# Kernel tuning notes

Measured on AMD Instinct MI355X. Metric: run time of the kernel, lower is better.

Reference implementation:

```python
import jax, jax.numpy as jnp
import numpy as np

DIM = 1024
HEADS = 16
DIM_HEAD = 64
INNER = HEADS * DIM_HEAD
SCALE = DIM_HEAD ** -0.5
LN_EPS = 1e-5
MASK_VALUE = -np.finfo(np.float32).max


def setup_inputs() -> dict:
    key = jax.random.key(0)
    ks = jax.random.split(key, 3)
    x = jax.random.normal(ks[0], (2, 2048, DIM), dtype=jnp.float32)
    w_qkv = jax.random.normal(ks[1], (DIM, 3 * INNER), dtype=jnp.float32) * (DIM ** -0.5)
    w_out = jax.random.normal(ks[2], (INNER, DIM), dtype=jnp.float32) * (INNER ** -0.5)
    ln_gamma = jnp.ones((DIM,), dtype=jnp.float32)
    ln_beta = jnp.zeros((DIM,), dtype=jnp.float32)
    return {"x": x, "ln_gamma": ln_gamma, "ln_beta": ln_beta, "w_qkv": w_qkv, "w_out": w_out}


def reference(x, ln_gamma, ln_beta, w_qkv, w_out):
    b, n, _ = x.shape
    # LayerNorm
    mu = jnp.mean(x, axis=-1, keepdims=True)
    var = jnp.mean(jnp.square(x - mu), axis=-1, keepdims=True)
    xn = (x - mu) * jax.lax.rsqrt(var + LN_EPS) * ln_gamma + ln_beta
    # QKV projection, split into heads: b n (h d) -> b h n d
    qkv = xn @ w_qkv  # [b, n, 3*inner]
    q, k, v = jnp.split(qkv, 3, axis=-1)
    def to_heads(t):
        return t.reshape(b, n, HEADS, DIM_HEAD).transpose(0, 2, 1, 3)
    q, k, v = to_heads(q), to_heads(k), to_heads(v)
    # scaled scores with diagonal excluded
    dots = jnp.einsum('bhnd,bhmd->bhnm', q, k) * SCALE
    eye = jnp.eye(n, dtype=bool)
    dots = jnp.where(eye, MASK_VALUE, dots)
    attn = jax.nn.softmax(dots, axis=-1)
    out = jnp.einsum('bhnm,bhmd->bhnd', attn, v)
    out = out.transpose(0, 2, 1, 3).reshape(b, n, INNER)
    return out @ w_out
```

## Files before the change

### kernel.cpp

```cpp
#include <hip/hip_runtime.h>


#define DIMM   1024
#define NSEQ   2048
#define BATCH  2
#define HEADS  16
#define DHEAD  64
#define QKVN   3072
#define MROWS  4096

typedef float          f32x4  __attribute__((ext_vector_type(4)));
typedef __bf16         bf16x8 __attribute__((ext_vector_type(8)));
typedef __bf16         bf16x4 __attribute__((ext_vector_type(4)));
typedef unsigned short u16x8  __attribute__((ext_vector_type(8)));
typedef unsigned short u16x4  __attribute__((ext_vector_type(4)));

#define QSCALE (0.125f * 1.4426950408889634f)

#if __has_builtin(__builtin_amdgcn_exp2f)
#define EXP2(x) __builtin_amdgcn_exp2f(x)
#else
#define EXP2(x) exp2f(x)
#endif

__device__ __forceinline__ unsigned short f2bf(float f) {
  unsigned u = __builtin_bit_cast(unsigned, f);
  u += 0x7FFFu + ((u >> 16) & 1u);
  return (unsigned short)(u >> 16);
}
__device__ __forceinline__ bf16x8 as_bf(u16x8 v) { return __builtin_bit_cast(bf16x8, v); }

__device__ __forceinline__ u16x4 cvt4(f32x4 v) {
  bf16x4 b;
  b[0] = (__bf16)v[0]; b[1] = (__bf16)v[1]; b[2] = (__bf16)v[2]; b[3] = (__bf16)v[3];
  return __builtin_bit_cast(u16x4, b);
}

__device__ __forceinline__ void gl_lds16(const unsigned short* g, unsigned short* l) {
  __builtin_amdgcn_global_load_lds(
      (const __attribute__((address_space(1))) unsigned*)g,
      (__attribute__((address_space(3))) unsigned*)l, 16, 0, 0);
}

__device__ __forceinline__ bf16x8 lds_frag(const unsigned short* base, int row, int chunk) {
  return as_bf(*(const u16x8*)&base[row * 64 + ((chunk ^ (row & 7)) << 3)]);
}

__device__ __forceinline__ void transpose_tile(
    const float* __restrict__ src, unsigned short* __restrict__ dst,
    int R, int C, int bx, int by, int tid) {
  __shared__ float t[32][33];
  const int rb = by * 32, cb = bx * 32;
  const int r0 = tid >> 5;
  const int c  = tid & 31;
#pragma unroll
  for (int i = 0; i < 4; ++i)
    t[r0 + i * 8][c] = src[(rb + r0 + i * 8) * C + cb + c];
  __syncthreads();
#pragma unroll
  for (int i = 0; i < 4; ++i)
    dst[(cb + r0 + i * 8) * R + rb + c] = f2bf(t[c][r0 + i * 8]);
}

__global__ __launch_bounds__(256) void prep_kernel(
    const float* __restrict__ x, const float* __restrict__ g,
    const float* __restrict__ be, const float* __restrict__ w_qkv,
    const float* __restrict__ w_out, unsigned short* __restrict__ xn,
    unsigned short* __restrict__ wqkvT, unsigned short* __restrict__ woutT) {
  const int bid = blockIdx.x, tid = threadIdx.x;
  if (bid < MROWS) {
    const int row = bid;
    const int wave = tid >> 6, lane = tid & 63;
    const float4 v = *(const float4*)&x[row * DIMM + tid * 4];
    float s  = v.x + v.y + v.z + v.w;
    float s2 = v.x * v.x + v.y * v.y + v.z * v.z + v.w * v.w;
#pragma unroll
    for (int o = 32; o >= 1; o >>= 1) { s += __shfl_xor(s, o); s2 += __shfl_xor(s2, o); }
    __shared__ float ps[4], ps2[4];
    if (lane == 0) { ps[wave] = s; ps2[wave] = s2; }
    __syncthreads();
    s  = ps[0] + ps[1] + ps[2] + ps[3];
    s2 = ps2[0] + ps2[1] + ps2[2] + ps2[3];
    const float mu  = s * (1.0f / DIMM);
    const float var = s2 * (1.0f / DIMM) - mu * mu;
    const float rs  = rsqrtf(var + 1e-5f);
    const float4 gg = *(const float4*)&g[tid * 4];
    const float4 bb = *(const float4*)&be[tid * 4];
    u16x4 o;
    o[0] = f2bf((v.x - mu) * rs * gg.x + bb.x);
    o[1] = f2bf((v.y - mu) * rs * gg.y + bb.y);
    o[2] = f2bf((v.z - mu) * rs * gg.z + bb.z);
    o[3] = f2bf((v.w - mu) * rs * gg.w + bb.w);
    *(u16x4*)&xn[row * DIMM + tid * 4] = o;
  } else {
    const int t = bid - MROWS;
    const int bx = t & 127, by = t >> 7;
    if (bx < QKVN / 32) transpose_tile(w_qkv, wqkvT, DIMM, QKVN, bx, by, tid);
    else                transpose_tile(w_out, woutT, DIMM, DIMM, bx - QKVN / 32, by, tid);
  }
}

__global__ __launch_bounds__(256, 3) void gemm_qkv_kernel(
    const unsigned short* __restrict__ A, const unsigned short* __restrict__ Bt,
    unsigned short* __restrict__ qb, unsigned short* __restrict__ kb,
    unsigned short* __restrict__ vtb) {
  __shared__ __attribute__((aligned(16))) unsigned short As[128 * 64];
  __shared__ __attribute__((aligned(16))) unsigned short Bs[128 * 64];
  const int tid = threadIdx.x;
  const int bm = blockIdx.y, bn = blockIdx.x;
  const int lane = tid & 63, wave = tid >> 6;
  const int l15 = lane & 15, quad = lane >> 4;
  const int wm = wave >> 1, wn = wave & 1;
  const int lrow = lane >> 3;
  const int gcol = ((lane & 7) ^ lrow) << 3;
  const unsigned short* Ab = A  + (bm * 128 + wave * 32 + lrow) * DIMM + gcol;
  const unsigned short* Bb = Bt + (bn * 128 + wave * 32 + lrow) * DIMM + gcol;
  const bool swap = (bn < 16);
  f32x4 acc[4][4] = {};

  for (int k0 = 0; k0 < DIMM; k0 += 64) {
#pragma unroll
    for (int j = 0; j < 4; ++j) {
      gl_lds16(Ab + j * 8 * DIMM + k0, &As[(wave * 32 + j * 8) * 64]);
      gl_lds16(Bb + j * 8 * DIMM + k0, &Bs[(wave * 32 + j * 8) * 64]);
    }
    __syncthreads();
#pragma unroll
    for (int kk = 0; kk < 2; ++kk) {
      bf16x8 af[4], bfr[4];
#pragma unroll
      for (int mi = 0; mi < 4; ++mi) af[mi]  = lds_frag(As, wm * 64 + mi * 16 + l15, kk * 4 + quad);
#pragma unroll
      for (int ni = 0; ni < 4; ++ni) bfr[ni] = lds_frag(Bs, wn * 64 + ni * 16 + l15, kk * 4 + quad);
      if (swap) {
#pragma unroll
        for (int mi = 0; mi < 4; ++mi)
#pragma unroll
          for (int ni = 0; ni < 4; ++ni)
            acc[mi][ni] = __builtin_amdgcn_mfma_f32_16x16x32_bf16(bfr[ni], af[mi], acc[mi][ni], 0, 0, 0);
      } else {
#pragma unroll
        for (int mi = 0; mi < 4; ++mi)
#pragma unroll
          for (int ni = 0; ni < 4; ++ni)
            acc[mi][ni] = __builtin_amdgcn_mfma_f32_16x16x32_bf16(af[mi], bfr[ni], acc[mi][ni], 0, 0, 0);
      }
    }
    __syncthreads();
  }

  if (swap) {
    const int colbase = bn * 128 + wn * 64;
    const int which = colbase >> 10;
    unsigned short* dst = which ? kb : qb;
    const float sc = which ? 1.0f : QSCALE;
#pragma unroll
    for (int mi = 0; mi < 4; ++mi) {
      const int m = bm * 128 + wm * 64 + mi * 16 + l15;
      const int bh0 = (m >> 11) * HEADS;
      const int n = m & 2047;
#pragma unroll
      for (int ni = 0; ni < 4; ++ni) {
        const int wc = (colbase & 1023) + ni * 16 + quad * 4;
        const int h = wc >> 6, dd = wc & 63;
        f32x4 v = acc[mi][ni] * sc;
        *(u16x4*)&dst[((bh0 + h) * NSEQ + n) * DHEAD + dd] = cvt4(v);
      }
    }
  } else {
    const int colbase = bn * 128 + wn * 64 - 2048;
#pragma unroll
    for (int mi = 0; mi < 4; ++mi) {
      const int m0 = bm * 128 + wm * 64 + mi * 16 + quad * 4;
      const int bh0 = (m0 >> 11) * HEADS;
      const int n0 = m0 & 2047;
#pragma unroll
      for (int ni = 0; ni < 4; ++ni) {
        const int vcol = colbase + ni * 16 + l15;
        const int h = vcol >> 6, dd = vcol & 63;
        *(u16x4*)&vtb[((bh0 + h) * DHEAD + dd) * NSEQ + n0] = cvt4(acc[mi][ni]);
      }
    }
  }
}

__global__ __launch_bounds__(512, 4) void attn_kernel(
    const unsigned short* __restrict__ qb, const unsigned short* __restrict__ kb,
    const unsigned short* __restrict__ vtb, unsigned short* __restrict__ attn_out) {
  __shared__ __attribute__((aligned(16))) unsigned short Ks[2][64 * 64];
  __shared__ __attribute__((aligned(16))) unsigned short Vts[2][64 * 64];
  __shared__ __attribute__((aligned(16))) unsigned short Ps[8][16][72];
  const int tid = threadIdx.x, wave = tid >> 6, lane = tid & 63;
  const int l15 = lane & 15, quad = lane >> 4;
  const int bh = blockIdx.x, qt = blockIdx.y;
  const int b = bh >> 4, h = bh & 15;
  const int qg = qt * 128 + wave * 16 + l15;

  bf16x8 aq[2];
  {
    const unsigned short* qrow = qb + (bh * NSEQ + qg) * DHEAD;
    aq[0] = as_bf(*(const u16x8*)(qrow + quad * 8));
    aq[1] = as_bf(*(const u16x8*)(qrow + 32 + quad * 8));
  }

  float lsum = 0.f;
  f32x4 occ[4] = {};

  const int lrow = lane >> 3;
  const int gcol = ((lane & 7) ^ lrow) << 3;
  const unsigned short* Kb = kb  + (bh * NSEQ + wave * 8 + lrow) * DHEAD + gcol;
  const unsigned short* Vb = vtb + (bh * DHEAD + wave * 8 + lrow) * NSEQ + gcol;

  gl_lds16(Kb, &Ks[0][(wave * 8) * 64]);
  gl_lds16(Vb, &Vts[0][(wave * 8) * 64]);

  const int diag_it = qt * 2 + (wave >> 2);
  const int kvo_want = (wave & 3) * 16 + l15;

  for (int it = 0; it < NSEQ / 64; ++it) {
    const int cur = it & 1;
    __syncthreads();
    if (it < NSEQ / 64 - 1) {
      gl_lds16(Kb + (it + 1) * 64 * DHEAD, &Ks[cur ^ 1][(wave * 8) * 64]);
      gl_lds16(Vb + (it + 1) * 64,         &Vts[cur ^ 1][(wave * 8) * 64]);
    }
    bf16x8 ak[2][4], av[2][4];
#pragma unroll
    for (int kk = 0; kk < 2; ++kk)
#pragma unroll
      for (int ct = 0; ct < 4; ++ct) {
        ak[kk][ct] = lds_frag(&Ks[cur][0],  ct * 16 + l15, kk * 4 + quad);
        av[kk][ct] = lds_frag(&Vts[cur][0], ct * 16 + l15, kk * 4 + quad);
      }
    f32x4 scc[4];
#pragma unroll
    for (int ct = 0; ct < 4; ++ct) scc[ct] = (f32x4){-32.f, -32.f, -32.f, -32.f};
#pragma unroll
    for (int kk = 0; kk < 2; ++kk)
#pragma unroll
      for (int ct = 0; ct < 4; ++ct)
        scc[ct] = __builtin_amdgcn_mfma_f32_16x16x32_bf16(ak[kk][ct], aq[kk], scc[ct], 0, 0, 0);
#pragma unroll
    for (int ct = 0; ct < 4; ++ct)
#pragma unroll
      for (int r = 0; r < 4; ++r) scc[ct][r] = EXP2(scc[ct][r]);

    if (it == diag_it) {
#pragma unroll
      for (int ct = 0; ct < 4; ++ct)
#pragma unroll
        for (int r = 0; r < 4; ++r)
          if (ct * 16 + quad * 4 + r == kvo_want) scc[ct][r] = 0.f;
    }

    f32x4 ps4 = (scc[0] + scc[1]) + (scc[2] + scc[3]);
    lsum += (ps4[0] + ps4[1]) + (ps4[2] + ps4[3]);

#pragma unroll
    for (int ct = 0; ct < 4; ++ct)
      *(u16x4*)&Ps[wave][l15][ct * 16 + quad * 4] = cvt4(scc[ct]);

#pragma unroll
    for (int kk = 0; kk < 2; ++kk) {
      bf16x8 bp = as_bf(*(const u16x8*)&Ps[wave][l15][kk * 32 + quad * 8]);
#pragma unroll
      for (int ct = 0; ct < 4; ++ct)
        occ[ct] = __builtin_amdgcn_mfma_f32_16x16x32_bf16(av[kk][ct], bp, occ[ct], 0, 0, 0);
    }
  }
  lsum += __shfl_xor(lsum, 16);
  lsum += __shfl_xor(lsum, 32);
  const float rl = __builtin_amdgcn_rcpf(lsum);
#pragma unroll
  for (int ct = 0; ct < 4; ++ct) {
    f32x4 ov = occ[ct] * rl;
    *(u16x4*)&attn_out[(b * NSEQ + qg) * DIMM + h * DHEAD + ct * 16 + quad * 4] = cvt4(ov);
  }
}

__global__ __launch_bounds__(256, 2) void gemm_out_kernel(
    const unsigned short* __restrict__ A,
    const unsigned short* __restrict__ Bt,
    float* __restrict__ out) {
  __shared__ __attribute__((aligned(16))) unsigned short As[2 * 64 * 64];
  __shared__ __attribute__((aligned(16))) unsigned short Bs[2 * 128 * 64];
  const int tid = threadIdx.x;
  const int bm = blockIdx.y, bn = blockIdx.x;
  const int lane = tid & 63, wave = tid >> 6;
  const int l15 = lane & 15, quad = lane >> 4;
  const int wm = wave >> 1, wn = wave & 1;
  const int lrow = lane >> 3;
  const int gcol = ((lane & 7) ^ lrow) << 3;
  const unsigned short* Ab = A  + (bm * 64 + wave * 16 + lrow) * DIMM + gcol;
  const unsigned short* Bb = Bt + (bn * 128 + wave * 32 + lrow) * DIMM + gcol;
  f32x4 acc[2][4] = {};

#pragma unroll
  for (int j = 0; j < 2; ++j) gl_lds16(Ab + j * 8 * DIMM, &As[(wave * 16 + j * 8) * 64]);
#pragma unroll
  for (int j = 0; j < 4; ++j) gl_lds16(Bb + j * 8 * DIMM, &Bs[(wave * 32 + j * 8) * 64]);

  for (int it = 0; it < DIMM / 64; ++it) {
    const int cur = it & 1;
    __syncthreads();
    if (it < DIMM / 64 - 1) {
      const int k0 = (it + 1) * 64;
      unsigned short* An = &As[(cur ^ 1) * 4096];
      unsigned short* Bn = &Bs[(cur ^ 1) * 8192];
#pragma unroll
      for (int j = 0; j < 2; ++j) gl_lds16(Ab + j * 8 * DIMM + k0, &An[(wave * 16 + j * 8) * 64]);
#pragma unroll
      for (int j = 0; j < 4; ++j) gl_lds16(Bb + j * 8 * DIMM + k0, &Bn[(wave * 32 + j * 8) * 64]);
    }
    const unsigned short* Ac = &As[cur * 4096];
    const unsigned short* Bc = &Bs[cur * 8192];
#pragma unroll
    for (int kk = 0; kk < 2; ++kk) {
      bf16x8 af[2], bfr[4];
#pragma unroll
      for (int mi = 0; mi < 2; ++mi) af[mi]  = lds_frag(Ac, wm * 32 + mi * 16 + l15, kk * 4 + quad);
#pragma unroll
      for (int ni = 0; ni < 4; ++ni) bfr[ni] = lds_frag(Bc, wn * 64 + ni * 16 + l15, kk * 4 + quad);
#pragma unroll
      for (int mi = 0; mi < 2; ++mi)
#pragma unroll
        for (int ni = 0; ni < 4; ++ni)
          acc[mi][ni] = __builtin_amdgcn_mfma_f32_16x16x32_bf16(bfr[ni], af[mi], acc[mi][ni], 0, 0, 0);
    }
  }
#pragma unroll
  for (int mi = 0; mi < 2; ++mi) {
    const int m = bm * 64 + wm * 32 + mi * 16 + l15;
#pragma unroll
    for (int ni = 0; ni < 4; ++ni) {
      const int col = bn * 128 + wn * 64 + ni * 16 + quad * 4;
      *(f32x4*)&out[m * DIMM + col] = acc[mi][ni];
    }
  }
}

extern "C" void kernel_launch(void* const* d_in, const int* in_sizes, int n_in,
                              void* d_out, int out_size, void* d_ws, size_t ws_size,
                              hipStream_t stream) {
  const float* x     = (const float*)d_in[0];
  const float* gamma = (const float*)d_in[1];
  const float* beta  = (const float*)d_in[2];
  const float* w_qkv = (const float*)d_in[3];
  const float* w_out = (const float*)d_in[4];
  float* out = (float*)d_out;

  char* ws = (char*)d_ws;
  unsigned short* xn    = (unsigned short*)(ws);
  unsigned short* wqkvT = (unsigned short*)(ws + 8388608);
  unsigned short* woutT = (unsigned short*)(ws + 14680064);
  unsigned short* qbuf  = (unsigned short*)(ws + 16777216);
  unsigned short* kbuf  = (unsigned short*)(ws + 25165824);
  unsigned short* vtbuf = (unsigned short*)(ws + 33554432);
  unsigned short* attnb = (unsigned short*)(ws + 41943040);

  prep_kernel<<<MROWS + (QKVN + DIMM) / 32 * (DIMM / 32), 256, 0, stream>>>(
      x, gamma, beta, w_qkv, w_out, xn, wqkvT, woutT);
  gemm_qkv_kernel<<<dim3(24, MROWS / 128), 256, 0, stream>>>(xn, wqkvT, qbuf, kbuf, vtbuf);
  attn_kernel<<<dim3(BATCH * HEADS, NSEQ / 128), 512, 0, stream>>>(qbuf, kbuf, vtbuf, attnb);
  gemm_out_kernel<<<dim3(DIMM / 128, MROWS / 64), 256, 0, stream>>>(attnb, woutT, out);
}
```

Baseline: 189.8 us.

## Process four 16-row query subtiles per wave in attention to reuse K/V fragments

Each attention wave now handles 64 query rows (four 16-row subtiles) instead of 16, and blocks shrink to 4 waves covering 256 queries. K and V fragments loaded from LDS are reused across the four subtiles, which cuts LDS reads and block-level syncs per unit of work. The cost is a larger register footprint (4x output accumulators and Q fragments) and half as many blocks (256), which reduces occupancy and parallelism.

```diff
diff --git a/kernel.cpp b/kernel.cpp
--- a/kernel.cpp
+++ b/kernel.cpp
@@ -184,45 +184,51 @@
   }
 }
 
-__global__ __launch_bounds__(512, 4) void attn_kernel(
+__global__ __launch_bounds__(256, 2) void attn_kernel(
     const unsigned short* __restrict__ qb, const unsigned short* __restrict__ kb,
     const unsigned short* __restrict__ vtb, unsigned short* __restrict__ attn_out) {
   __shared__ __attribute__((aligned(16))) unsigned short Ks[2][64 * 64];
   __shared__ __attribute__((aligned(16))) unsigned short Vts[2][64 * 64];
-  __shared__ __attribute__((aligned(16))) unsigned short Ps[8][16][72];
+  __shared__ __attribute__((aligned(16))) unsigned short Ps[4][16][72];
   const int tid = threadIdx.x, wave = tid >> 6, lane = tid & 63;
   const int l15 = lane & 15, quad = lane >> 4;
   const int bh = blockIdx.x, qt = blockIdx.y;
   const int b = bh >> 4, h = bh & 15;
-  const int qg = qt * 128 + wave * 16 + l15;
-
-  bf16x8 aq[2];
-  {
-    const unsigned short* qrow = qb + (bh * NSEQ + qg) * DHEAD;
-    aq[0] = as_bf(*(const u16x8*)(qrow + quad * 8));
-    aq[1] = as_bf(*(const u16x8*)(qrow + 32 + quad * 8));
-  }
-
-  float lsum = 0.f;
-  f32x4 occ[4] = {};
+  const int qbase = qt * 256 + wave * 64;
+
+  bf16x8 aq[4][2];
+#pragma unroll
+  for (int sub = 0; sub < 4; ++sub) {
+    const unsigned short* qrow = qb + (bh * NSEQ + qbase + sub * 16 + l15) * DHEAD;
+    aq[sub][0] = as_bf(*(const u16x8*)(qrow + quad * 8));
+    aq[sub][1] = as_bf(*(const u16x8*)(qrow + 32 + quad * 8));
+  }
+
+  float lsum[4] = {};
+  f32x4 occ[4][4] = {};
 
   const int lrow = lane >> 3;
   const int gcol = ((lane & 7) ^ lrow) << 3;
-  const unsigned short* Kb = kb  + (bh * NSEQ + wave * 8 + lrow) * DHEAD + gcol;
-  const unsigned short* Vb = vtb + (bh * DHEAD + wave * 8 + lrow) * NSEQ + gcol;
-
-  gl_lds16(Kb, &Ks[0][(wave * 8) * 64]);
-  gl_lds16(Vb, &Vts[0][(wave * 8) * 64]);
-
-  const int diag_it = qt * 2 + (wave >> 2);
-  const int kvo_want = (wave & 3) * 16 + l15;
+  const unsigned short* Kb = kb  + (bh * NSEQ + wave * 16 + lrow) * DHEAD + gcol;
+  const unsigned short* Vb = vtb + (bh * DHEAD + wave * 16 + lrow) * NSEQ + gcol;
+
+  gl_lds16(Kb,             &Ks[0][(wave * 16) * 64]);
+  gl_lds16(Kb + 8 * DHEAD, &Ks[0][(wave * 16 + 8) * 64]);
+  gl_lds16(Vb,             &Vts[0][(wave * 16) * 64]);
+  gl_lds16(Vb + 8 * NSEQ,  &Vts[0][(wave * 16 + 8) * 64]);
+
+  const int diag_it = qt * 4 + wave;
+  const bool diag_lane = ((l15 >> 2) == quad);
+  const int diag_r = l15 & 3;
 
   for (int it = 0; it < NSEQ / 64; ++it) {
     const int cur = it & 1;
     __syncthreads();
     if (it < NSEQ / 64 - 1) {
-      gl_lds16(Kb + (it + 1) * 64 * DHEAD, &Ks[cur ^ 1][(wave * 8) * 64]);
-      gl_lds16(Vb + (it + 1) * 64,         &Vts[cur ^ 1][(wave * 8) * 64]);
+      gl_lds16(Kb + (it + 1) * 64 * DHEAD,             &Ks[cur ^ 1][(wave * 16) * 64]);
+      gl_lds16(Kb + (it + 1) * 64 * DHEAD + 8 * DHEAD, &Ks[cur ^ 1][(wave * 16 + 8) * 64]);
+      gl_lds16(Vb + (it + 1) * 64,                     &Vts[cur ^ 1][(wave * 16) * 64]);
+      gl_lds16(Vb + (it + 1) * 64 + 8 * NSEQ,          &Vts[cur ^ 1][(wave * 16 + 8) * 64]);
     }
     bf16x8 ak[2][4], av[2][4];
 #pragma unroll
@@ -232,49 +238,51 @@
         ak[kk][ct] = lds_frag(&Ks[cur][0],  ct * 16 + l15, kk * 4 + quad);
         av[kk][ct] = lds_frag(&Vts[cur][0], ct * 16 + l15, kk * 4 + quad);
       }
-    f32x4 scc[4];
-#pragma unroll
-    for (int ct = 0; ct < 4; ++ct) scc[ct] = (f32x4){-32.f, -32.f, -32.f, -32.f};
-#pragma unroll
-    for (int kk = 0; kk < 2; ++kk)
+#pragma unroll
+    for (int sub = 0; sub < 4; ++sub) {
+      f32x4 scc[4];
+#pragma unroll
+      for (int ct = 0; ct < 4; ++ct) scc[ct] = (f32x4){-32.f, -32.f, -32.f, -32.f};
+#pragma unroll
+      for (int kk = 0; kk < 2; ++kk)
+#pragma unroll
+        for (int ct = 0; ct < 4; ++ct)
+          scc[ct] = __builtin_amdgcn_mfma_f32_16x16x32_bf16(ak[kk][ct], aq[sub][kk], scc[ct], 0, 0, 0);
 #pragma unroll
       for (int ct = 0; ct < 4; ++ct)
-        scc[ct] = __builtin_amdgcn_mfma_f32_16x16x32_bf16(ak[kk][ct], aq[kk], scc[ct], 0, 0, 0);
-#pragma unroll
-    for (int ct = 0; ct < 4; ++ct)
-#pragma unroll
-      for (int r = 0; r < 4; ++r) scc[ct][r] = EXP2(scc[ct][r]);
-
-    if (it == diag_it) {
+#pragma unroll
+        for (int r = 0; r < 4; ++r) scc[ct][r] = EXP2(scc[ct][r]);
+
+      if (it == diag_it && diag_lane) scc[sub][diag_r] = 0.f;
+
+      f32x4 ps4 = (scc[0] + scc[1]) + (scc[2] + scc[3]);
+      lsum[sub] += (ps4[0] + ps4[1]) + (ps4[2] + ps4[3]);
+
 #pragma unroll
       for (int ct = 0; ct < 4; ++ct)
-#pragma unroll
-        for (int r = 0; r < 4; ++r)
-          if (ct * 16 + quad * 4 + r == kvo_want) scc[ct][r] = 0.f;
-    }
-
-    f32x4 ps4 = (scc[0] + scc[1]) + (scc[2] + scc[3]);
-    lsum += (ps4[0] + ps4[1]) + (ps4[2] + ps4[3]);
-
-#pragma unroll
-    for (int ct = 0; ct < 4; ++ct)
-      *(u16x4*)&Ps[wave][l15][ct * 16 + quad * 4] = cvt4(scc[ct]);
-
-#pragma unroll
-    for (int kk = 0; kk < 2; ++kk) {
-      bf16x8 bp = as_bf(*(const u16x8*)&Ps[wave][l15][kk * 32 + quad * 8]);
-#pragma unroll
-      for (int ct = 0; ct < 4; ++ct)
-        occ[ct] = __builtin_amdgcn_mfma_f32_16x16x32_bf16(av[kk][ct], bp, occ[ct], 0, 0, 0);
-    }
-  }
-  lsum += __shfl_xor(lsum, 16);
-  lsum += __shfl_xor(lsum, 32);
-  const float rl = __builtin_amdgcn_rcpf(lsum);
-#pragma unroll
-  for (int ct = 0; ct < 4; ++ct) {
-    f32x4 ov = occ[ct] * rl;
-    *(u16x4*)&attn_out[(b * NSEQ + qg) * DIMM + h * DHEAD + ct * 16 + quad * 4] = cvt4(ov);
+        *(u16x4*)&Ps[wave][l15][ct * 16 + quad * 4] = cvt4(scc[ct]);
+
+#pragma unroll
+      for (int kk = 0; kk < 2; ++kk) {
+        bf16x8 bp = as_bf(*(const u16x8*)&Ps[wave][l15][kk * 32 + quad * 8]);
+#pragma unroll
+        for (int ct = 0; ct < 4; ++ct)
+          occ[sub][ct] = __builtin_amdgcn_mfma_f32_16x16x32_bf16(av[kk][ct], bp, occ[sub][ct], 0, 0, 0);
+      }
+    }
+  }
+#pragma unroll
+  for (int sub = 0; sub < 4; ++sub) {
+    float l = lsum[sub];
+    l += __shfl_xor(l, 16);
+    l += __shfl_xor(l, 32);
+    const float rl = __builtin_amdgcn_rcpf(l);
+    const int qg = qbase + sub * 16 + l15;
+#pragma unroll
+    for (int ct = 0; ct < 4; ++ct) {
+      f32x4 ov = occ[sub][ct] * rl;
+      *(u16x4*)&attn_out[(b * NSEQ + qg) * DIMM + h * DHEAD + ct * 16 + quad * 4] = cvt4(ov);
+    }
   }
 }
 
@@ -361,6 +369,6 @@
   prep_kernel<<<MROWS + (QKVN + DIMM) / 32 * (DIMM / 32), 256, 0, stream>>>(
       x, gamma, beta, w_qkv, w_out, xn, wqkvT, woutT);
   gemm_qkv_kernel<<<dim3(24, MROWS / 128), 256, 0, stream>>>(xn, wqkvT, qbuf, kbuf, vtbuf);
-  attn_kernel<<<dim3(BATCH * HEADS, NSEQ / 128), 512, 0, stream>>>(qbuf, kbuf, vtbuf, attnb);
+  attn_kernel<<<dim3(BATCH * HEADS, NSEQ / 256), 256, 0, stream>>>(qbuf, kbuf, vtbuf, attnb);
   gemm_out_kernel<<<dim3(DIMM / 128, MROWS / 64), 256, 0, stream>>>(attnb, woutT, out);
 }
```

Result: slower. 201.1 us (+5.9%).
